# Kernel optimization log

Hardware: AMD Instinct MI355X
Metric: run time of the kernel (lower is better)

The kernel has to match this reference:

```python
import jax, jax.numpy as jnp
import numpy as np


def setup_inputs() -> dict:
    key = jax.random.key(0)
    ks = jax.random.split(key, 6)
    b, c, h, w = 4, 64, 64, 64
    hid = 32
    x = jax.random.normal(ks[0], (b, c, h, w), dtype=jnp.float32)
    sc_in = 1.0 / np.sqrt(c)
    sc_hid = 1.0 / np.sqrt(hid)
    wq = jax.random.normal(ks[1], (hid, c), dtype=jnp.float32) * sc_in
    wk = jax.random.normal(ks[2], (hid, c), dtype=jnp.float32) * sc_in
    wv = jax.random.normal(ks[3], (hid, c), dtype=jnp.float32) * sc_in
    wp = jax.random.normal(ks[4], (c, hid), dtype=jnp.float32) * sc_hid
    bq = jnp.zeros((hid,), jnp.float32)
    bk = jnp.zeros((hid,), jnp.float32)
    bv = jnp.zeros((hid,), jnp.float32)
    bp = jnp.zeros((c,), jnp.float32)
    return {"x": x, "wq": wq, "bq": bq, "wk": wk, "bk": bk,
            "wv": wv, "bv": bv, "wp": wp, "bp": bp}


def reference(x, wq, bq, wk, bk, wv, bv, wp, bp):
    b, c, h, w = x.shape
    hid = wq.shape[0]
    # flatten spatial: [b, c, n]
    xf = x.reshape(b, c, h * w)
    # 1x1 convs == channel linear: q,k,v are [b, hid, n]
    q = jnp.einsum('oc,bcn->bon', wq, xf) + bq[None, :, None]
    k = jnp.einsum('oc,bcn->bon', wk, xf) + bk[None, :, None]
    v = jnp.einsum('oc,bcn->bon', wv, xf) + bv[None, :, None]
    # attention scores: query [b,n,hid] @ key [b,hid,m] -> [b,n,m] (NO scaling, as in source)
    scores = jnp.einsum('bhn,bhm->bnm', q, k)
    attn = jax.nn.softmax(scores, axis=-1)
    # z = attn @ value^T -> [b, n, hid] -> [b, hid, n]
    z = jnp.einsum('bnm,bhm->bhn', attn, v)
    # output projection (1x1 conv) + residual
    out = xf + jnp.einsum('ch,bhn->bcn', wp, z) + bp[None, :, None]
    return out.reshape(b, c, h, w)
```

## Files before the change

### kernel.cpp

```cpp
#include <hip/hip_runtime.h>
#include <hip/hip_bf16.h>
#include <math.h>

#define BB 4
#define CC 64
#define HID 32
#define NN 4096
#define LOG2E 1.44269504088896f

typedef short sh2 __attribute__((ext_vector_type(2)));
typedef short sh8 __attribute__((ext_vector_type(8)));
typedef float f2v __attribute__((ext_vector_type(2)));
typedef float f4v __attribute__((ext_vector_type(4)));

#define MFMA32(A,B,C) __builtin_amdgcn_mfma_f32_16x16x32_bf16(A,B,C,0,0,0)

__device__ __forceinline__ short f2b(float f) {
    __hip_bfloat16 h = __float2bfloat16(f);
    union { __hip_bfloat16 hb; short s; } u; u.hb = h; return u.s;
}

__global__ __launch_bounds__(1024) void qkv_kernel(
    const float* __restrict__ x,
    const float* __restrict__ wq, const float* __restrict__ bq,
    const float* __restrict__ wk, const float* __restrict__ bk,
    const float* __restrict__ wv, const float* __restrict__ bv,
    short* __restrict__ Qw, short* __restrict__ Kw, short* __restrict__ Vtp)
{
    __shared__ float xs[64][84];
    __shared__ float ws[96][84];
    __shared__ float bs[96];

    const int t  = threadIdx.x;
    const int b  = blockIdx.x >> 6;
    const int n0 = (blockIdx.x & 63) << 6;

    {
        int c = t >> 4, j4 = (t & 15) << 2;
        *(f4v*)&xs[c][j4] = *(const f4v*)(x + ((size_t)(b*CC + c))*NN + n0 + j4);
    }
    #pragma unroll
    for (int kl = 0; kl < 2; ++kl) {
        int idx = t + 1024*kl;
        if (idx < 1536) {
            int r = idx >> 4, c4 = (idx & 15) << 2;
            const float* src = (r < 32) ? (wq + r*CC + c4)
                             : (r < 64) ? (wk + (r-32)*CC + c4)
                                        : (wv + (r-64)*CC + c4);
            *(f4v*)&ws[r][c4] = *(const f4v*)src;
        }
    }
    if (t < 96) bs[t] = (t < 32) ? bq[t] : (t < 64) ? bk[t-32] : bv[t-64];
    __syncthreads();

    const int hg = t & 31;
    const int j0 = (t >> 5) << 1;

    float aq[2], ak[2], av[2];
    #pragma unroll
    for (int jj = 0; jj < 2; ++jj) { aq[jj]=bs[hg]; ak[jj]=bs[32+hg]; av[jj]=bs[64+hg]; }

    #pragma unroll
    for (int cs = 0; cs < 16; ++cs) {
        f4v wqv = *(f4v*)&ws[hg][cs*4];
        f4v wkv = *(f4v*)&ws[32+hg][cs*4];
        f4v wvv = *(f4v*)&ws[64+hg][cs*4];
        #pragma unroll
        for (int cc = 0; cc < 4; ++cc) {
            f2v xv = *(f2v*)&xs[cs*4+cc][j0];
            #pragma unroll
            for (int jj = 0; jj < 2; ++jj) {
                aq[jj] += wqv[cc]*xv[jj];
                ak[jj] += wkv[cc]*xv[jj];
                av[jj] += wvv[cc]*xv[jj];
            }
        }
    }

    const size_t nbase = (size_t)b*NN + n0 + j0;
    #pragma unroll
    for (int jj = 0; jj < 2; ++jj) {
        Qw[(nbase + jj)*HID + hg] = f2b(aq[jj] * LOG2E);
        Kw[(nbase + jj)*HID + hg] = f2b(ak[jj]);
    }
    const int w0  = j0 & 31;
    const int pos = 8*((w0 >> 2) & 3) + (w0 & 3) + 4*(w0 >> 4);
    sh2 vv; vv[0] = f2b(av[0]); vv[1] = f2b(av[1]);
    *(sh2*)(Vtp + ((size_t)b*HID + hg)*NN + n0 + (j0 & ~31) + pos) = vv;
}

__global__ __launch_bounds__(1024, 4) void attn_kernel(
    const short* __restrict__ Qw, const short* __restrict__ Kw,
    const short* __restrict__ Vtp, const float* __restrict__ x,
    const float* __restrict__ wp, const float* __restrict__ bp,
    float* __restrict__ out)
{
    __shared__ float zr[8][64][33];
    __shared__ float lr[8][64];

    const int t    = threadIdx.x;
    const int b    = blockIdx.x >> 6;
    const int q0   = (blockIdx.x & 63) << 6;
    const int lane = t & 63;
    const int w    = t >> 6;
    const int g    = lane >> 4;
    const int qi   = lane & 15;

    sh8 qf[4];
    #pragma unroll
    for (int S = 0; S < 4; ++S)
        qf[S] = *(const sh8*)(Qw + ((size_t)b*NN + q0 + S*16 + qi)*HID + 8*g);

    const short* kp = Kw  + ((size_t)b*NN  + w*256 + qi)*HID + 8*g;
    const short* vp = Vtp + ((size_t)b*HID + qi)*NN + w*256 + 8*g;

    const f4v zf = {0.f,0.f,0.f,0.f};
    f4v z0[4], z1[4];
    float lacc[4];
    #pragma unroll
    for (int S = 0; S < 4; ++S) { z0[S] = zf; z1[S] = zf; lacc[S] = 0.f; }

    sh8 a0 = *(const sh8*)kp;
    sh8 a1 = *(const sh8*)(kp + 512);
    sh8 v0 = *(const sh8*)vp;
    sh8 v1 = *(const sh8*)(vp + 16*NN);

    for (int it = 0; it < 8; ++it) {
        const int nx = (it < 7) ? it + 1 : it;
        const short* kn = kp + (size_t)nx*1024;
        const short* vn = vp + (size_t)nx*32;
        sh8 na0 = *(const sh8*)kn;
        sh8 na1 = *(const sh8*)(kn + 512);
        sh8 nv0 = *(const sh8*)vn;
        sh8 nv1 = *(const sh8*)(vn + 16*NN);

        f4v s0[4], s1[4];
        #pragma unroll
        for (int S = 0; S < 4; ++S) {
            s0[S] = MFMA32(a0, qf[S], zf);
            s1[S] = MFMA32(a1, qf[S], zf);
        }

        sh8 p[4];
        #pragma unroll
        for (int S = 0; S < 4; ++S) {
            float e[8];
            #pragma unroll
            for (int r = 0; r < 4; ++r) {
                e[r]   = __builtin_amdgcn_exp2f(s0[S][r]);
                e[4+r] = __builtin_amdgcn_exp2f(s1[S][r]);
            }
            lacc[S] += ((e[0]+e[1])+(e[2]+e[3])) + ((e[4]+e[5])+(e[6]+e[7]));
            #pragma unroll
            for (int j = 0; j < 8; ++j) p[S][j] = f2b(e[j]);
        }

        #pragma unroll
        for (int S = 0; S < 4; ++S) {
            z0[S] = MFMA32(v0, p[S], z0[S]);
            z1[S] = MFMA32(v1, p[S], z1[S]);
        }

        a0 = na0; a1 = na1; v0 = nv0; v1 = nv1;
    }

    #pragma unroll
    for (int S = 0; S < 4; ++S) {
        lacc[S] += __shfl_xor(lacc[S], 16, 64);
        lacc[S] += __shfl_xor(lacc[S], 32, 64);
    }

    if (w >= 8) {
        #pragma unroll
        for (int S = 0; S < 4; ++S) {
            *(f4v*)&zr[w-8][S*16 + qi][4*g]      = z0[S];
            *(f4v*)&zr[w-8][S*16 + qi][16 + 4*g] = z1[S];
            if (g == 0) lr[w-8][S*16 + qi] = lacc[S];
        }
    }
    __syncthreads();
    if (w < 8) {
        #pragma unroll
        for (int S = 0; S < 4; ++S) {
            f4v ta = *(f4v*)&zr[w][S*16 + qi][4*g];
            f4v tb = *(f4v*)&zr[w][S*16 + qi][16 + 4*g];
            ta += z0[S]; tb += z1[S];
            *(f4v*)&zr[w][S*16 + qi][4*g]      = ta;
            *(f4v*)&zr[w][S*16 + qi][16 + 4*g] = tb;
            if (g == 0) lr[w][S*16 + qi] += lacc[S];
        }
    }
    __syncthreads();

    if (w < 4) {
        const int q = w*16 + qi;
        float lm = 0.f;
        #pragma unroll
        for (int s = 0; s < 8; ++s) lm += lr[s][q];
        f4v zm0 = zf, zm1 = zf;
        #pragma unroll
        for (int s = 0; s < 8; ++s) {
            zm0 += *(f4v*)&zr[s][q][4*g];
            zm1 += *(f4v*)&zr[s][q][16 + 4*g];
        }
        const float inv = 1.f / lm;
        sh8 pz;
        #pragma unroll
        for (int r = 0; r < 4; ++r) {
            pz[r]   = f2b(zm0[r]*inv);
            pz[4+r] = f2b(zm1[r]*inv);
        }
        const int qcol = q0 + q;
        #pragma unroll
        for (int ct = 0; ct < 4; ++ct) {
            const float* wrow = wp + (ct*16 + qi)*HID;
            f4v wa = *(const f4v*)(wrow + 4*g);
            f4v wb = *(const f4v*)(wrow + 16 + 4*g);
            sh8 af;
            #pragma unroll
            for (int i = 0; i < 4; ++i) { af[i] = f2b(wa[i]); af[4+i] = f2b(wb[i]); }
            f4v cacc;
            #pragma unroll
            for (int r = 0; r < 4; ++r) {
                int c = ct*16 + 4*g + r;
                cacc[r] = x[((size_t)(b*CC + c))*NN + qcol] + bp[c];
            }
            cacc = MFMA32(af, pz, cacc);
            #pragma unroll
            for (int r = 0; r < 4; ++r) {
                int c = ct*16 + 4*g + r;
                out[((size_t)(b*CC + c))*NN + qcol] = cacc[r];
            }
        }
    }
}

extern "C" void kernel_launch(void* const* d_in, const int* in_sizes, int n_in,
                              void* d_out, int out_size, void* d_ws, size_t ws_size,
                              hipStream_t stream) {
    const float* x  = (const float*)d_in[0];
    const float* wq = (const float*)d_in[1];
    const float* bq = (const float*)d_in[2];
    const float* wk = (const float*)d_in[3];
    const float* bk = (const float*)d_in[4];
    const float* wv = (const float*)d_in[5];
    const float* bv = (const float*)d_in[6];
    const float* wp = (const float*)d_in[7];
    const float* bp = (const float*)d_in[8];

    short* Qw  = (short*)d_ws;
    short* Kw  = Qw + (size_t)BB*NN*HID;
    short* Vtp = Kw + (size_t)BB*NN*HID;

    qkv_kernel<<<dim3(256), dim3(1024), 0, stream>>>(x, wq, bq, wk, bk, wv, bv, Qw, Kw, Vtp);
    attn_kernel<<<dim3(256), dim3(1024), 0, stream>>>(Qw, Kw, Vtp, x, wp, bp, (float*)d_out);
}
```

Before: 30.09 us.

## Halve query tile per block and double-buffer K/V loads with inline asm

After: 41.71 us. 1.39x slower.

```diff
diff --git a/kernel.cpp b/kernel.cpp
--- a/kernel.cpp
+++ b/kernel.cpp
@@ -19,6 +19,14 @@
     __hip_bfloat16 h = __float2bfloat16(f);
     union { __hip_bfloat16 hb; short s; } u; u.hb = h; return u.s;
 }
+
+__device__ __forceinline__ sh8 gload16(const short* p) {
+    sh8 r;
+    asm volatile("global_load_dwordx4 %0, %1, off" : "=v"(r) : "v"(p));
+    return r;
+}
+#define VMWAIT(N) do { asm volatile("s_waitcnt vmcnt(" #N ")" ::: "memory"); \
+                       __builtin_amdgcn_sched_barrier(0); } while (0)
 
 __global__ __launch_bounds__(1024) void qkv_kernel(
     const float* __restrict__ x,
@@ -95,105 +103,111 @@
     const float* __restrict__ wp, const float* __restrict__ bp,
     float* __restrict__ out)
 {
-    __shared__ float zr[8][64][33];
-    __shared__ float lr[8][64];
+    __shared__ float zr[8][32][33];
+    __shared__ float lr[8][32];
 
     const int t    = threadIdx.x;
-    const int b    = blockIdx.x >> 6;
-    const int q0   = (blockIdx.x & 63) << 6;
+    const int b    = blockIdx.x >> 7;
+    const int q0   = (blockIdx.x & 127) << 5;
     const int lane = t & 63;
     const int w    = t >> 6;
     const int g    = lane >> 4;
     const int qi   = lane & 15;
 
-    sh8 qf[4];
-    #pragma unroll
-    for (int S = 0; S < 4; ++S)
-        qf[S] = *(const sh8*)(Qw + ((size_t)b*NN + q0 + S*16 + qi)*HID + 8*g);
-
-    const short* kp = Kw  + ((size_t)b*NN  + w*256 + qi)*HID + 8*g;
-    const short* vp = Vtp + ((size_t)b*HID + qi)*NN + w*256 + 8*g;
+    const sh8 qf0 = *(const sh8*)(Qw + ((size_t)b*NN + q0 + qi)*HID + 8*g);
+    const sh8 qf1 = *(const sh8*)(Qw + ((size_t)b*NN + q0 + 16 + qi)*HID + 8*g);
+
+    const short* kbase  = Kw  + ((size_t)b*NN  + w*256 + qi)*HID + 8*g;
+    const short* vbase0 = Vtp + ((size_t)b*HID + qi)*NN + w*256 + 8*g;
+    const short* vbase1 = vbase0 + 16*NN;
 
     const f4v zf = {0.f,0.f,0.f,0.f};
-    f4v z0[4], z1[4];
-    float lacc[4];
-    #pragma unroll
-    for (int S = 0; S < 4; ++S) { z0[S] = zf; z1[S] = zf; lacc[S] = 0.f; }
-
-    sh8 a0 = *(const sh8*)kp;
-    sh8 a1 = *(const sh8*)(kp + 512);
-    sh8 v0 = *(const sh8*)vp;
-    sh8 v1 = *(const sh8*)(vp + 16*NN);
-
-    for (int it = 0; it < 8; ++it) {
-        const int nx = (it < 7) ? it + 1 : it;
-        const short* kn = kp + (size_t)nx*1024;
-        const short* vn = vp + (size_t)nx*32;
-        sh8 na0 = *(const sh8*)kn;
-        sh8 na1 = *(const sh8*)(kn + 512);
-        sh8 nv0 = *(const sh8*)vn;
-        sh8 nv1 = *(const sh8*)(vn + 16*NN);
-
-        f4v s0[4], s1[4];
-        #pragma unroll
-        for (int S = 0; S < 4; ++S) {
-            s0[S] = MFMA32(a0, qf[S], zf);
-            s1[S] = MFMA32(a1, qf[S], zf);
-        }
-
-        sh8 p[4];
-        #pragma unroll
-        for (int S = 0; S < 4; ++S) {
-            float e[8];
-            #pragma unroll
-            for (int r = 0; r < 4; ++r) {
-                e[r]   = __builtin_amdgcn_exp2f(s0[S][r]);
-                e[4+r] = __builtin_amdgcn_exp2f(s1[S][r]);
-            }
-            lacc[S] += ((e[0]+e[1])+(e[2]+e[3])) + ((e[4]+e[5])+(e[6]+e[7]));
-            #pragma unroll
-            for (int j = 0; j < 8; ++j) p[S][j] = f2b(e[j]);
-        }
-
-        #pragma unroll
-        for (int S = 0; S < 4; ++S) {
-            z0[S] = MFMA32(v0, p[S], z0[S]);
-            z1[S] = MFMA32(v1, p[S], z1[S]);
-        }
-
-        a0 = na0; a1 = na1; v0 = nv0; v1 = nv1;
-    }
-
-    #pragma unroll
-    for (int S = 0; S < 4; ++S) {
-        lacc[S] += __shfl_xor(lacc[S], 16, 64);
-        lacc[S] += __shfl_xor(lacc[S], 32, 64);
-    }
+    f4v z00 = zf, z01 = zf, z10 = zf, z11 = zf;
+    float lacc0 = 0.f, lacc1 = 0.f;
+
+    asm volatile("s_waitcnt vmcnt(0)" ::: "memory");
+
+    sh8 aA0 = gload16(kbase);
+    sh8 aA1 = gload16(kbase + 512);
+    sh8 vA0 = gload16(vbase0);
+    sh8 vA1 = gload16(vbase1);
+    sh8 aB0 = gload16(kbase + 1024);
+    sh8 aB1 = gload16(kbase + 1536);
+    sh8 vB0 = gload16(vbase0 + 32);
+    sh8 vB1 = gload16(vbase1 + 32);
+
+#define BODY(A0,A1,V0,V1,T,ISSUE)                                          \
+    {                                                                      \
+        f4v s0a = MFMA32(A0, qf0, zf);                                     \
+        f4v s1a = MFMA32(A1, qf0, zf);                                     \
+        f4v s0b = MFMA32(A0, qf1, zf);                                     \
+        f4v s1b = MFMA32(A1, qf1, zf);                                     \
+        if (ISSUE) {                                                       \
+            A0 = gload16(kbase + (T+2)*1024);                              \
+            A1 = gload16(kbase + (T+2)*1024 + 512);                        \
+        }                                                                  \
+        float e0[8], e1[8];                                                \
+        _Pragma("unroll")                                                  \
+        for (int r = 0; r < 4; ++r) {                                      \
+            e0[r]   = __builtin_amdgcn_exp2f(s0a[r]);                      \
+            e0[4+r] = __builtin_amdgcn_exp2f(s1a[r]);                      \
+            e1[r]   = __builtin_amdgcn_exp2f(s0b[r]);                      \
+            e1[4+r] = __builtin_amdgcn_exp2f(s1b[r]);                      \
+        }                                                                  \
+        lacc0 += ((e0[0]+e0[1])+(e0[2]+e0[3])) + ((e0[4]+e0[5])+(e0[6]+e0[7])); \
+        lacc1 += ((e1[0]+e1[1])+(e1[2]+e1[3])) + ((e1[4]+e1[5])+(e1[6]+e1[7])); \
+        sh8 p0, p1;                                                        \
+        _Pragma("unroll")                                                  \
+        for (int j = 0; j < 8; ++j) { p0[j] = f2b(e0[j]); p1[j] = f2b(e1[j]); } \
+        z00 = MFMA32(V0, p0, z00);                                         \
+        z01 = MFMA32(V1, p0, z01);                                         \
+        z10 = MFMA32(V0, p1, z10);                                         \
+        z11 = MFMA32(V1, p1, z11);                                         \
+        if (ISSUE) {                                                       \
+            V0 = gload16(vbase0 + (T+2)*32);                               \
+            V1 = gload16(vbase1 + (T+2)*32);                               \
+        }                                                                  \
+    }
+
+    VMWAIT(4); BODY(aA0,aA1,vA0,vA1, 0, 1);
+    VMWAIT(4); BODY(aB0,aB1,vB0,vB1, 1, 1);
+    VMWAIT(4); BODY(aA0,aA1,vA0,vA1, 2, 1);
+    VMWAIT(4); BODY(aB0,aB1,vB0,vB1, 3, 1);
+    VMWAIT(4); BODY(aA0,aA1,vA0,vA1, 4, 1);
+    VMWAIT(4); BODY(aB0,aB1,vB0,vB1, 5, 1);
+    VMWAIT(4); BODY(aA0,aA1,vA0,vA1, 6, 0);
+    VMWAIT(0); BODY(aB0,aB1,vB0,vB1, 7, 0);
+#undef BODY
+
+    lacc0 += __shfl_xor(lacc0, 16, 64);  lacc0 += __shfl_xor(lacc0, 32, 64);
+    lacc1 += __shfl_xor(lacc1, 16, 64);  lacc1 += __shfl_xor(lacc1, 32, 64);
 
     if (w >= 8) {
-        #pragma unroll
-        for (int S = 0; S < 4; ++S) {
-            *(f4v*)&zr[w-8][S*16 + qi][4*g]      = z0[S];
-            *(f4v*)&zr[w-8][S*16 + qi][16 + 4*g] = z1[S];
-            if (g == 0) lr[w-8][S*16 + qi] = lacc[S];
-        }
+        const int s = w - 8;
+        *(f4v*)&zr[s][qi][4*g]           = z00;
+        *(f4v*)&zr[s][qi][16 + 4*g]      = z01;
+        *(f4v*)&zr[s][16 + qi][4*g]      = z10;
+        *(f4v*)&zr[s][16 + qi][16 + 4*g] = z11;
+        if (g == 0) { lr[s][qi] = lacc0; lr[s][16 + qi] = lacc1; }
     }
     __syncthreads();
     if (w < 8) {
-        #pragma unroll
-        for (int S = 0; S < 4; ++S) {
-            f4v ta = *(f4v*)&zr[w][S*16 + qi][4*g];
-            f4v tb = *(f4v*)&zr[w][S*16 + qi][16 + 4*g];
-            ta += z0[S]; tb += z1[S];
-            *(f4v*)&zr[w][S*16 + qi][4*g]      = ta;
-            *(f4v*)&zr[w][S*16 + qi][16 + 4*g] = tb;
-            if (g == 0) lr[w][S*16 + qi] += lacc[S];
-        }
+        f4v t00 = *(f4v*)&zr[w][qi][4*g]           + z00;
+        f4v t01 = *(f4v*)&zr[w][qi][16 + 4*g]      + z01;
+        f4v t10 = *(f4v*)&zr[w][16 + qi][4*g]      + z10;
+        f4v t11 = *(f4v*)&zr[w][16 + qi][16 + 4*g] + z11;
+        *(f4v*)&zr[w][qi][4*g]           = t00;
+        *(f4v*)&zr[w][qi][16 + 4*g]      = t01;
+        *(f4v*)&zr[w][16 + qi][4*g]      = t10;
+        *(f4v*)&zr[w][16 + qi][16 + 4*g] = t11;
+        if (g == 0) { lr[w][qi] += lacc0; lr[w][16 + qi] += lacc1; }
     }
     __syncthreads();
 
-    if (w < 4) {
-        const int q = w*16 + qi;
+    if (w < 8) {
+        const int S  = w & 1;
+        const int ct = w >> 1;
+        const int q  = S*16 + qi;
         float lm = 0.f;
         #pragma unroll
         for (int s = 0; s < 8; ++s) lm += lr[s][q];
@@ -211,26 +225,23 @@
             pz[4+r] = f2b(zm1[r]*inv);
         }
         const int qcol = q0 + q;
-        #pragma unroll
-        for (int ct = 0; ct < 4; ++ct) {
-            const float* wrow = wp + (ct*16 + qi)*HID;
-            f4v wa = *(const f4v*)(wrow + 4*g);
-            f4v wb = *(const f4v*)(wrow + 16 + 4*g);
-            sh8 af;
-            #pragma unroll
-            for (int i = 0; i < 4; ++i) { af[i] = f2b(wa[i]); af[4+i] = f2b(wb[i]); }
-            f4v cacc;
-            #pragma unroll
-            for (int r = 0; r < 4; ++r) {
-                int c = ct*16 + 4*g + r;
-                cacc[r] = x[((size_t)(b*CC + c))*NN + qcol] + bp[c];
-            }
-            cacc = MFMA32(af, pz, cacc);
-            #pragma unroll
-            for (int r = 0; r < 4; ++r) {
-                int c = ct*16 + 4*g + r;
-                out[((size_t)(b*CC + c))*NN + qcol] = cacc[r];
-            }
+        const float* wrow = wp + (ct*16 + qi)*HID;
+        f4v wa = *(const f4v*)(wrow + 4*g);
+        f4v wb = *(const f4v*)(wrow + 16 + 4*g);
+        sh8 af;
+        #pragma unroll
+        for (int i = 0; i < 4; ++i) { af[i] = f2b(wa[i]); af[4+i] = f2b(wb[i]); }
+        f4v cacc;
+        #pragma unroll
+        for (int r = 0; r < 4; ++r) {
+            int c = ct*16 + 4*g + r;
+            cacc[r] = x[((size_t)(b*CC + c))*NN + qcol] + bp[c];
+        }
+        cacc = MFMA32(af, pz, cacc);
+        #pragma unroll
+        for (int r = 0; r < 4; ++r) {
+            int c = ct*16 + 4*g + r;
+            out[((size_t)(b*CC + c))*NN + qcol] = cacc[r];
         }
     }
 }
@@ -253,5 +264,5 @@
     short* Vtp = Kw + (size_t)BB*NN*HID;
 
     qkv_kernel<<<dim3(256), dim3(1024), 0, stream>>>(x, wq, bq, wk, bk, wv, bv, Qw, Kw, Vtp);
-    attn_kernel<<<dim3(256), dim3(1024), 0, stream>>>(Qw, Kw, Vtp, x, wp, bp, (float*)d_out);
-}
+    attn_kernel<<<dim3(512), dim3(1024), 0, stream>>>(Qw, Kw, Vtp, x, wp, bp, (float*)d_out);
+}
```

## Halve attention block to 8 waves with two interleaved key chains per wave

Applied to the files above, without the earlier changes.

After: 33.06 us. 9.9% more time.

```diff
diff --git a/kernel.cpp b/kernel.cpp
--- a/kernel.cpp
+++ b/kernel.cpp
@@ -89,20 +89,20 @@
     *(sh2*)(Vtp + ((size_t)b*HID + hg)*NN + n0 + (j0 & ~31) + pos) = vv;
 }
 
-__global__ __launch_bounds__(1024, 4) void attn_kernel(
+__global__ __launch_bounds__(512, 2) void attn_kernel(
     const short* __restrict__ Qw, const short* __restrict__ Kw,
     const short* __restrict__ Vtp, const float* __restrict__ x,
     const float* __restrict__ wp, const float* __restrict__ bp,
     float* __restrict__ out)
 {
-    __shared__ float zr[8][64][33];
-    __shared__ float lr[8][64];
+    __shared__ float zr[4][32][65];
+    __shared__ float lr4[4][64];
 
     const int t    = threadIdx.x;
     const int b    = blockIdx.x >> 6;
     const int q0   = (blockIdx.x & 63) << 6;
     const int lane = t & 63;
-    const int w    = t >> 6;
+    const int kq   = t >> 6;
     const int g    = lane >> 4;
     const int qi   = lane & 15;
 
@@ -111,8 +111,8 @@
     for (int S = 0; S < 4; ++S)
         qf[S] = *(const sh8*)(Qw + ((size_t)b*NN + q0 + S*16 + qi)*HID + 8*g);
 
-    const short* kp = Kw  + ((size_t)b*NN  + w*256 + qi)*HID + 8*g;
-    const short* vp = Vtp + ((size_t)b*HID + qi)*NN + w*256 + 8*g;
+    const short* kp = Kw  + ((size_t)b*NN  + kq*512 + qi)*HID + 8*g;
+    const short* vp = Vtp + ((size_t)b*HID + qi)*NN + kq*512 + 8*g;
 
     const f4v zf = {0.f,0.f,0.f,0.f};
     f4v z0[4], z1[4];
@@ -120,49 +120,59 @@
     #pragma unroll
     for (int S = 0; S < 4; ++S) { z0[S] = zf; z1[S] = zf; lacc[S] = 0.f; }
 
-    sh8 a0 = *(const sh8*)kp;
-    sh8 a1 = *(const sh8*)(kp + 512);
-    sh8 v0 = *(const sh8*)vp;
-    sh8 v1 = *(const sh8*)(vp + 16*NN);
-
+    sh8 aA0 = *(const sh8*)(kp);
+    sh8 aA1 = *(const sh8*)(kp + 512);
+    sh8 vA0 = *(const sh8*)(vp);
+    sh8 vA1 = *(const sh8*)(vp + 16*NN);
+    sh8 aB0 = *(const sh8*)(kp + 1024);
+    sh8 aB1 = *(const sh8*)(kp + 1536);
+    sh8 vB0 = *(const sh8*)(vp + 32);
+    sh8 vB1 = *(const sh8*)(vp + 32 + 16*NN);
+
+#define CHAIN(A0,A1,V0,V1,KOFF,VOFF,IT)                                     \
+    {                                                                       \
+        sh8 n0, n1, m0, m1;                                                 \
+        if ((IT) < 7) {                                                     \
+            const short* kn = kp + (size_t)((IT)+1)*2048 + (KOFF);          \
+            const short* vn = vp + (size_t)((IT)+1)*64 + (VOFF);            \
+            n0 = *(const sh8*)kn;                                           \
+            n1 = *(const sh8*)(kn + 512);                                   \
+            m0 = *(const sh8*)vn;                                           \
+            m1 = *(const sh8*)(vn + 16*NN);                                 \
+        }                                                                   \
+        f4v s0[4], s1[4];                                                   \
+        _Pragma("unroll")                                                   \
+        for (int S = 0; S < 4; ++S) {                                       \
+            s0[S] = MFMA32(A0, qf[S], zf);                                  \
+            s1[S] = MFMA32(A1, qf[S], zf);                                  \
+        }                                                                   \
+        sh8 p[4];                                                           \
+        _Pragma("unroll")                                                   \
+        for (int S = 0; S < 4; ++S) {                                       \
+            float e[8];                                                     \
+            _Pragma("unroll")                                               \
+            for (int r = 0; r < 4; ++r) {                                   \
+                e[r]   = __builtin_amdgcn_exp2f(s0[S][r]);                  \
+                e[4+r] = __builtin_amdgcn_exp2f(s1[S][r]);                  \
+            }                                                               \
+            lacc[S] += ((e[0]+e[1])+(e[2]+e[3])) + ((e[4]+e[5])+(e[6]+e[7]));\
+            _Pragma("unroll")                                               \
+            for (int j = 0; j < 8; ++j) p[S][j] = f2b(e[j]);                \
+        }                                                                   \
+        _Pragma("unroll")                                                   \
+        for (int S = 0; S < 4; ++S) {                                       \
+            z0[S] = MFMA32(V0, p[S], z0[S]);                                \
+            z1[S] = MFMA32(V1, p[S], z1[S]);                                \
+        }                                                                   \
+        if ((IT) < 7) { A0 = n0; A1 = n1; V0 = m0; V1 = m1; }               \
+    }
+
+    #pragma unroll 2
     for (int it = 0; it < 8; ++it) {
-        const int nx = (it < 7) ? it + 1 : it;
-        const short* kn = kp + (size_t)nx*1024;
-        const short* vn = vp + (size_t)nx*32;
-        sh8 na0 = *(const sh8*)kn;
-        sh8 na1 = *(const sh8*)(kn + 512);
-        sh8 nv0 = *(const sh8*)vn;
-        sh8 nv1 = *(const sh8*)(vn + 16*NN);
-
-        f4v s0[4], s1[4];
-        #pragma unroll
-        for (int S = 0; S < 4; ++S) {
-            s0[S] = MFMA32(a0, qf[S], zf);
-            s1[S] = MFMA32(a1, qf[S], zf);
-        }
-
-        sh8 p[4];
-        #pragma unroll
-        for (int S = 0; S < 4; ++S) {
-            float e[8];
-            #pragma unroll
-            for (int r = 0; r < 4; ++r) {
-                e[r]   = __builtin_amdgcn_exp2f(s0[S][r]);
-                e[4+r] = __builtin_amdgcn_exp2f(s1[S][r]);
-            }
-            lacc[S] += ((e[0]+e[1])+(e[2]+e[3])) + ((e[4]+e[5])+(e[6]+e[7]));
-            #pragma unroll
-            for (int j = 0; j < 8; ++j) p[S][j] = f2b(e[j]);
-        }
-
-        #pragma unroll
-        for (int S = 0; S < 4; ++S) {
-            z0[S] = MFMA32(v0, p[S], z0[S]);
-            z1[S] = MFMA32(v1, p[S], z1[S]);
-        }
-
-        a0 = na0; a1 = na1; v0 = nv0; v1 = nv1;
-    }
+        CHAIN(aA0, aA1, vA0, vA1, 0,    0,  it);
+        CHAIN(aB0, aB1, vB0, vB1, 1024, 32, it);
+    }
+#undef CHAIN
 
     #pragma unroll
     for (int S = 0; S < 4; ++S) {
@@ -170,38 +180,42 @@
         lacc[S] += __shfl_xor(lacc[S], 32, 64);
     }
 
-    if (w >= 8) {
+    if (kq >= 4) {
         #pragma unroll
         for (int S = 0; S < 4; ++S) {
-            *(f4v*)&zr[w-8][S*16 + qi][4*g]      = z0[S];
-            *(f4v*)&zr[w-8][S*16 + qi][16 + 4*g] = z1[S];
-            if (g == 0) lr[w-8][S*16 + qi] = lacc[S];
+            #pragma unroll
+            for (int r = 0; r < 4; ++r) {
+                zr[kq-4][4*g+r][S*16+qi]    = z0[S][r];
+                zr[kq-4][16+4*g+r][S*16+qi] = z1[S][r];
+            }
+            if (g == 0) lr4[kq-4][S*16+qi] = lacc[S];
         }
     }
     __syncthreads();
-    if (w < 8) {
+    if (kq < 4) {
         #pragma unroll
         for (int S = 0; S < 4; ++S) {
-            f4v ta = *(f4v*)&zr[w][S*16 + qi][4*g];
-            f4v tb = *(f4v*)&zr[w][S*16 + qi][16 + 4*g];
-            ta += z0[S]; tb += z1[S];
-            *(f4v*)&zr[w][S*16 + qi][4*g]      = ta;
-            *(f4v*)&zr[w][S*16 + qi][16 + 4*g] = tb;
-            if (g == 0) lr[w][S*16 + qi] += lacc[S];
+            #pragma unroll
+            for (int r = 0; r < 4; ++r) {
+                zr[kq][4*g+r][S*16+qi]    += z0[S][r];
+                zr[kq][16+4*g+r][S*16+qi] += z1[S][r];
+            }
+            if (g == 0) lr4[kq][S*16+qi] += lacc[S];
         }
     }
     __syncthreads();
 
-    if (w < 4) {
-        const int q = w*16 + qi;
-        float lm = 0.f;
-        #pragma unroll
-        for (int s = 0; s < 8; ++s) lm += lr[s][q];
+    if (kq < 4) {
+        const int q = kq*16 + qi;
+        float lm = (lr4[0][q] + lr4[1][q]) + (lr4[2][q] + lr4[3][q]);
         f4v zm0 = zf, zm1 = zf;
         #pragma unroll
-        for (int s = 0; s < 8; ++s) {
-            zm0 += *(f4v*)&zr[s][q][4*g];
-            zm1 += *(f4v*)&zr[s][q][16 + 4*g];
+        for (int j = 0; j < 4; ++j) {
+            #pragma unroll
+            for (int r = 0; r < 4; ++r) {
+                zm0[r] += zr[j][4*g+r][q];
+                zm1[r] += zr[j][16+4*g+r][q];
+            }
         }
         const float inv = 1.f / lm;
         sh8 pz;
@@ -253,5 +267,5 @@
     short* Vtp = Kw + (size_t)BB*NN*HID;
 
     qkv_kernel<<<dim3(256), dim3(1024), 0, stream>>>(x, wq, bq, wk, bk, wv, bv, Qw, Kw, Vtp);
-    attn_kernel<<<dim3(256), dim3(1024), 0, stream>>>(Qw, Kw, Vtp, x, wp, bp, (float*)d_out);
-}
+    attn_kernel<<<dim3(256), dim3(512), 0, stream>>>(Qw, Kw, Vtp, x, wp, bp, (float*)d_out);
+}
```
